# Kernel optimization log

Measured on AMD Instinct MI355X. Metric: run time of the kernel, lower is better.

## Reference

```python
import jax, jax.numpy as jnp
import numpy as np

B, S, D, H = 2, 2048, 1024, 16
DEPTH = D // H


def setup_inputs() -> dict:
    key = jax.random.key(0)
    ks = jax.random.split(key, 6)
    q = jax.random.normal(ks[0], (B, S, D), dtype=jnp.float32)
    k = jax.random.normal(ks[1], (B, S, D), dtype=jnp.float32)
    v = jax.random.normal(ks[2], (B, S, D), dtype=jnp.float32)
    # causal mask, broadcastable to [B, H, S, S]
    mask = jnp.tril(jnp.ones((S, S), dtype=bool))[None, None, :, :]
    wq = jax.random.normal(ks[3], (D, D), dtype=jnp.float32)
    wk = jax.random.normal(ks[4], (D, D), dtype=jnp.float32)
    wv = jax.random.normal(ks[5], (D, D), dtype=jnp.float32)
    return {"q": q, "k": k, "v": v, "mask": mask, "wq": wq, "wk": wk, "wv": wv}


def _split_heads(x):
    # [B, S, D] -> [B, H, S, depth]
    return x.reshape(x.shape[0], -1, H, DEPTH).transpose(0, 2, 1, 3)


def reference(q, k, v, mask, wq, wk, wv):
    q = _split_heads(q @ wq)
    k = _split_heads(k @ wk)
    v = _split_heads(v @ wv)
    scale = jnp.sqrt(jnp.float32(DEPTH))
    # [B, H, S, S]
    scores = jnp.einsum("bhqd,bhkd->bhqk", q, k) / scale
    scores = jnp.where(mask, scores, jnp.float32(-8.0))
    scores = scores - jnp.max(scores, axis=-1, keepdims=True)
    attn = jax.nn.softmax(scores, axis=-1)
    out = jnp.einsum("bhqk,bhkd->bhqd", attn, v)
    # [B, H, S, depth] -> [B, S, D]
    return out.transpose(0, 2, 1, 3).reshape(out.shape[0], -1, D)
```

## Files before the change

kernel.cpp:

```cpp
#include <hip/hip_runtime.h>
#include <hip/hip_bf16.h>

#define B_  2
#define S_  2048
#define D_  1024
#define H_  16
#define DH_ 64

typedef __attribute__((ext_vector_type(8)))  short  short8;
typedef __attribute__((ext_vector_type(4)))  short  short4b;
typedef __attribute__((ext_vector_type(16))) float  f32x16;

#define MFMA32(A,B,C) __builtin_amdgcn_mfma_f32_32x32x16_bf16(A,B,C,0,0,0)

static __device__ __forceinline__ short bf16b(float x) {
    __hip_bfloat16 h = __float2bfloat16(x);
    return *(short*)&h;
}
static __device__ __forceinline__ float bf16tof(short s) {
    union { unsigned u; float f; } cv;
    cv.u = ((unsigned)(unsigned short)s) << 16;
    return cv.f;
}
static __device__ __forceinline__ void gl2lds(const short* g, short* l) {
    __builtin_amdgcn_global_load_lds(
        (const __attribute__((address_space(1))) unsigned int*)g,
        (__attribute__((address_space(3))) unsigned int*)l, 16, 0, 0);
}
static __device__ __forceinline__ unsigned cvtpk(float a, float b) {
    unsigned r;
    asm("v_cvt_pk_bf16_f32 %0, %1, %2" : "=v"(r) : "v"(a), "v"(b));
    return r;
}
static __device__ __forceinline__ void pl32swap(unsigned &a, unsigned &b) {
    asm volatile("v_permlane32_swap_b32 %0, %1" : "+v"(a), "+v"(b));
}

__global__ __launch_bounds__(256)
void conv_all(const float* __restrict__ q, const float* __restrict__ k,
              const float* __restrict__ v,
              const float* __restrict__ wq, const float* __restrict__ wk,
              const float* __restrict__ wv, char* __restrict__ ws) {
    __shared__ short HiT[64][80];
    __shared__ short LoT[64][80];
    const int bid = blockIdx.x;
    const int t   = threadIdx.x;
    if (bid < 12288) {
        const int z   = bid >> 12;
        const int xb  = bid & 4095;
        const float* src = z == 0 ? q : z == 1 ? k : v;
        short* hi = (short*)(ws + (size_t)z * 16777216);
        short* lo = hi + 4194304;
        const int i = (xb * 256 + t) * 4;
        float4 xv = *(const float4*)&src[i];
        const float* xf = (const float*)&xv;
        short4b h4, l4;
#pragma unroll
        for (int e = 0; e < 4; ++e) {
            short hb = bf16b(xf[e]);
            h4[e] = hb;
            l4[e] = bf16b(xf[e] - bf16tof(hb));
        }
        *(short4b*)&hi[i] = h4;
        *(short4b*)&lo[i] = l4;
        return;
    }
    const int wid = bid - 12288;
    const int z   = wid >> 8;
    const int rem = wid & 255;
    const int k0  = (rem & 15) << 6, n0 = (rem >> 4) << 6;
    const float* w = z == 0 ? wq : z == 1 ? wk : wv;
    short* oh = (short*)(ws + 50331648 + (size_t)z * 4194304);
    short* ol = oh + 1048576;

    const int kr = t >> 2, c4 = (t & 3) * 16;
    const float* srow = w + (size_t)(k0 + kr) * 1024 + n0 + c4;
#pragma unroll
    for (int u = 0; u < 16; u += 4) {
        float4 f = *(const float4*)&srow[u];
        const float* ff = (const float*)&f;
#pragma unroll
        for (int e = 0; e < 4; ++e) {
            int nl = c4 + u + e;
            short hb = bf16b(ff[e]);
            HiT[nl][kr] = hb;
            LoT[nl][kr] = bf16b(ff[e] - bf16tof(hb));
        }
    }
    __syncthreads();
    const int nl = t >> 2, kc = (t & 3) * 16;
    size_t off = (size_t)(n0 + nl) * 1024 + k0 + kc;
    *(short8*)&oh[off]     = *(const short8*)&HiT[nl][kc];
    *(short8*)&oh[off + 8] = *(const short8*)&HiT[nl][kc + 8];
    *(short8*)&ol[off]     = *(const short8*)&LoT[nl][kc];
    *(short8*)&ol[off + 8] = *(const short8*)&LoT[nl][kc + 8];
}

#define QAH_ 0
#define QAL_ 4096
#define QBH_ 8192
#define QBL_ 12288

__global__ __launch_bounds__(512, 2)
void proj_mfma(const short* __restrict__ xh0, const short* __restrict__ xl0,
               const short* __restrict__ xh1, const short* __restrict__ xl1,
               const short* __restrict__ xh2, const short* __restrict__ xl2,
               const short* __restrict__ wh0, const short* __restrict__ wl0,
               const short* __restrict__ wh1, const short* __restrict__ wl1,
               const short* __restrict__ wh2, const short* __restrict__ wl2,
               short* __restrict__ qh, short* __restrict__ ql,
               short* __restrict__ kh, short* __restrict__ kl,
               short* __restrict__ vt) {
    __shared__ __align__(16) short lds[65536];
    const int z  = blockIdx.z;
    const int m0 = blockIdx.y * 256;
    const int n0 = blockIdx.x * 256;
    const int t = threadIdx.x, lane = t & 63, w = t >> 6;
    const int l31 = lane & 31, hh = lane >> 5;
    const int wr = w >> 2, wc = w & 3;

    const short* xh = z == 0 ? xh0 : z == 1 ? xh1 : xh2;
    const short* xl = z == 0 ? xl0 : z == 1 ? xl1 : xl2;
    const short* wh = z == 0 ? wh0 : z == 1 ? wh1 : wh2;
    const short* wl = z == 0 ? wl0 : z == 1 ? wl1 : wl2;

    const int c    = (w << 6) | lane;
    const int rowS = c >> 1, pq = c & 1;
    const int pqs8 = (pq ^ ((rowS >> 2) & 1)) * 8;
    const short* gAh = xh + (size_t)(m0 + rowS) * 1024 + pqs8;
    const short* gAl = xl + (size_t)(m0 + rowS) * 1024 + pqs8;
    const short* gBh = wh + (size_t)(n0 + rowS) * 1024 + pqs8;
    const short* gBl = wl + (size_t)(n0 + rowS) * 1024 + pqs8;
    const int wS = w << 9;

    const int co = ((hh ^ ((l31 >> 2) & 1)) << 3);
    int rA[4], rB[2];
#pragma unroll
    for (int p = 0; p < 4; ++p) rA[p] = (wr * 128 + p * 32 + l31) * 16 + co;
#pragma unroll
    for (int n = 0; n < 2; ++n) rB[n] = (wc * 64 + n * 32 + l31) * 16 + co;

    f32x16 acc[4][2] = {};

    gl2lds(gAh,      &lds[QAH_ + wS]);
    gl2lds(gBh,      &lds[QBH_ + wS]);
    gl2lds(gAl,      &lds[QAL_ + wS]);
    gl2lds(gBl,      &lds[QBL_ + wS]);
    gl2lds(gAh + 16, &lds[16384 + QAH_ + wS]);
    gl2lds(gBh + 16, &lds[16384 + QBH_ + wS]);
    gl2lds(gAl + 16, &lds[16384 + QAL_ + wS]);
    gl2lds(gBl + 16, &lds[16384 + QBL_ + wS]);
    asm volatile("s_waitcnt vmcnt(4)" ::: "memory");
    __builtin_amdgcn_s_barrier();

#define PHASE_MFMA(PA, PB)                                                    \
    acc[PA][0] = MFMA32(ah0, bh0k, acc[PA][0]);                               \
    acc[PA][1] = MFMA32(ah0, bh1k, acc[PA][1]);                               \
    acc[PB][0] = MFMA32(ah1, bh0k, acc[PB][0]);                               \
    acc[PB][1] = MFMA32(ah1, bh1k, acc[PB][1]);                               \
    acc[PA][0] = MFMA32(ah0, bl0k, acc[PA][0]);                               \
    acc[PA][1] = MFMA32(ah0, bl1k, acc[PA][1]);                               \
    acc[PB][0] = MFMA32(ah1, bl0k, acc[PB][0]);                               \
    acc[PB][1] = MFMA32(ah1, bl1k, acc[PB][1]);                               \
    acc[PA][0] = MFMA32(al0, bh0k, acc[PA][0]);                               \
    acc[PA][1] = MFMA32(al0, bh1k, acc[PA][1]);                               \
    acc[PB][0] = MFMA32(al1, bh0k, acc[PB][0]);                               \
    acc[PB][1] = MFMA32(al1, bh1k, acc[PB][1]);

    for (int kt = 0; kt < 32; ++kt) {
        const int tb = (kt & 1) << 15;
        const int nb = 32768 - tb;
        const int nk = (kt + 1) * 32;
        const bool st = (kt < 31);

        short8 bh0k, bh1k, bl0k, bl1k, ah0, ah1, al0, al1;

        __builtin_amdgcn_sched_barrier(0);
        bh0k = *(const short8*)&lds[tb + QBH_ + rB[0]];
        bh1k = *(const short8*)&lds[tb + QBH_ + rB[1]];
        bl0k = *(const short8*)&lds[tb + QBL_ + rB[0]];
        bl1k = *(const short8*)&lds[tb + QBL_ + rB[1]];
        ah0  = *(const short8*)&lds[tb + QAH_ + rA[0]];
        ah1  = *(const short8*)&lds[tb + QAH_ + rA[1]];
        al0  = *(const short8*)&lds[tb + QAL_ + rA[0]];
        al1  = *(const short8*)&lds[tb + QAL_ + rA[1]];
        if (st) { gl2lds(gAh + nk, &lds[nb + QAH_ + wS]);
                  gl2lds(gBh + nk, &lds[nb + QBH_ + wS]); }
        __builtin_amdgcn_s_barrier();
        asm volatile("s_waitcnt lgkmcnt(0)" ::: "memory");
        __builtin_amdgcn_sched_barrier(0);
        __builtin_amdgcn_s_setprio(1);
        PHASE_MFMA(0, 1)
        __builtin_amdgcn_s_setprio(0);
        __builtin_amdgcn_sched_barrier(0);
        __builtin_amdgcn_s_barrier();

        __builtin_amdgcn_sched_barrier(0);
        ah0 = *(const short8*)&lds[tb + QAH_ + rA[2]];
        ah1 = *(const short8*)&lds[tb + QAH_ + rA[3]];
        al0 = *(const short8*)&lds[tb + QAL_ + rA[2]];
        al1 = *(const short8*)&lds[tb + QAL_ + rA[3]];
        if (st) { gl2lds(gAl + nk, &lds[nb + QAL_ + wS]);
                  gl2lds(gBl + nk, &lds[nb + QBL_ + wS]);
                  asm volatile("s_waitcnt vmcnt(4)" ::: "memory");
        } else {  asm volatile("s_waitcnt vmcnt(0)" ::: "memory"); }
        __builtin_amdgcn_s_barrier();
        asm volatile("s_waitcnt lgkmcnt(0)" ::: "memory");
        __builtin_amdgcn_sched_barrier(0);
        __builtin_amdgcn_s_setprio(1);
        PHASE_MFMA(2, 3)
        __builtin_amdgcn_s_setprio(0);
        __builtin_amdgcn_sched_barrier(0);
        __builtin_amdgcn_s_barrier();

        __builtin_amdgcn_sched_barrier(0);
        bh0k = *(const short8*)&lds[tb + 16384 + QBH_ + rB[0]];
        bh1k = *(const short8*)&lds[tb + 16384 + QBH_ + rB[1]];
        bl0k = *(const short8*)&lds[tb + 16384 + QBL_ + rB[0]];
        bl1k = *(const short8*)&lds[tb + 16384 + QBL_ + rB[1]];
        ah0  = *(const short8*)&lds[tb + 16384 + QAH_ + rA[0]];
        ah1  = *(const short8*)&lds[tb + 16384 + QAH_ + rA[1]];
        al0  = *(const short8*)&lds[tb + 16384 + QAL_ + rA[0]];
        al1  = *(const short8*)&lds[tb + 16384 + QAL_ + rA[1]];
        if (st) { gl2lds(gAh + nk + 16, &lds[nb + 16384 + QAH_ + wS]);
                  gl2lds(gBh + nk + 16, &lds[nb + 16384 + QBH_ + wS]); }
        __builtin_amdgcn_s_barrier();
        asm volatile("s_waitcnt lgkmcnt(0)" ::: "memory");
        __builtin_amdgcn_sched_barrier(0);
        __builtin_amdgcn_s_setprio(1);
        PHASE_MFMA(0, 1)
        __builtin_amdgcn_s_setprio(0);
        __builtin_amdgcn_sched_barrier(0);
        __builtin_amdgcn_s_barrier();

        __builtin_amdgcn_sched_barrier(0);
        ah0 = *(const short8*)&lds[tb + 16384 + QAH_ + rA[2]];
        ah1 = *(const short8*)&lds[tb + 16384 + QAH_ + rA[3]];
        al0 = *(const short8*)&lds[tb + 16384 + QAL_ + rA[2]];
        al1 = *(const short8*)&lds[tb + 16384 + QAL_ + rA[3]];
        if (st) { gl2lds(gAl + nk + 16, &lds[nb + 16384 + QAL_ + wS]);
                  gl2lds(gBl + nk + 16, &lds[nb + 16384 + QBL_ + wS]);
                  asm volatile("s_waitcnt vmcnt(4)" ::: "memory"); }
        __builtin_amdgcn_s_barrier();
        asm volatile("s_waitcnt lgkmcnt(0)" ::: "memory");
        __builtin_amdgcn_sched_barrier(0);
        __builtin_amdgcn_s_setprio(1);
        PHASE_MFMA(2, 3)
        __builtin_amdgcn_s_setprio(0);
        __builtin_amdgcn_sched_barrier(0);
        __builtin_amdgcn_s_barrier();
    }
#undef PHASE_MFMA

    const int bb = m0 >> 11;
    const int sbase = (m0 & 2047) + wr * 128;
    if (z < 2) {
        short* oh = z == 0 ? qh : kh;
        short* ol = z == 0 ? ql : kl;
        const float qs = (z == 0) ? 0.125f : 1.0f;
#pragma unroll
        for (int p = 0; p < 4; ++p)
#pragma unroll
        for (int nt = 0; nt < 2; ++nt) {
            int n_g = n0 + wc * 64 + nt * 32 + l31;
            int h = n_g >> 6, d = n_g & 63;
#pragma unroll
            for (int r = 0; r < 16; ++r) {
                int s = sbase + p * 32 + (r & 3) + 8 * (r >> 2) + 4 * hh;
                size_t off = (((size_t)(bb * 16 + h) * 2048 + s) << 6) + d;
                float a = acc[p][nt][r] * qs;
                short hb = bf16b(a);
                oh[off] = hb;
                ol[off] = bf16b(a - bf16tof(hb));
            }
        }
    } else {
#pragma unroll
        for (int p = 0; p < 4; ++p)
#pragma unroll
        for (int nt = 0; nt < 2; ++nt) {
            int n_g = n0 + wc * 64 + nt * 32 + l31;
            int h = n_g >> 6, d = n_g & 63;
            size_t vbase = ((size_t)(bb * 16 + h) * 64 + d) * 2048;
#pragma unroll
            for (int r2 = 0; r2 < 4; ++r2) {
                int s0 = sbase + p * 32 + 8 * r2 + 4 * hh;
                short4b pk;
#pragma unroll
                for (int a2 = 0; a2 < 4; ++a2)
                    pk[a2] = bf16b(acc[p][nt][r2 * 4 + a2]);
                *(short4b*)&vt[vbase + s0] = pk;
            }
        }
    }
}

__global__ __launch_bounds__(256, 2)
void attn_mfma(const short* __restrict__ Qhi, const short* __restrict__ Qlo,
               const short* __restrict__ Khi, const short* __restrict__ Klo,
               const short* __restrict__ Vt,  float* __restrict__ out) {
    __shared__ __align__(16) short SBUF[24576];
    __shared__ float svp[4][64];
    __shared__ float svs[64];
#define KhiS (SBUF)
#define KloS (SBUF + 8192)
#define VtS  (SBUF + 16384)

    const int t     = threadIdx.x;
    const int lane  = t & 63;
    const int w     = t >> 6;
    const int l31   = lane & 31;
    const int hh    = lane >> 5;
    const int bh    = blockIdx.x;
    const int yy    = blockIdx.y;
    const int qt    = (yy < 8) ? yy : 23 - yy;
    const int q0    = qt * 128;
    const int myq   = q0 + w * 32 + l31;
    const int myq_min = q0 + w * 32;
    const int ktend = 2 * qt + 2;

    const size_t basebh = (size_t)bh * S_ * DH_;

    {
        const int s_begin = ktend * 64;
        float part = 0.f;
        const short* vrow = Vt + basebh + (size_t)lane * S_;
        for (int s = s_begin + w * 8; s < S_; s += 32) {
            short8 vv = *(const short8*)&vrow[s];
#pragma unroll
            for (int e = 0; e < 8; ++e) part += bf16tof(vv[e]);
        }
        svp[w][lane] = part;
    }
    __syncthreads();
    if (t < 64)
        svs[t] = svp[0][t] + svp[1][t] + svp[2][t] + svp[3][t];

    short8 qh[4], ql[4];
    {
        const short* qr = Qhi + basebh + (size_t)myq * DH_;
        const short* lr = Qlo + basebh + (size_t)myq * DH_;
#pragma unroll
        for (int kf = 0; kf < 4; ++kf) {
            int dofs = kf * 16 + hh * 8;
            qh[kf] = *(const short8*)(qr + dofs);
            ql[kf] = *(const short8*)(lr + dofs);
        }
    }

    const int i1 = (w << 6) | lane;
    const int i2 = 256 + i1;
    const int r1 = i1 >> 3, c1 = (i1 & 7) ^ (r1 & 7);
    const int r2 = i2 >> 3, c2 = (i2 & 7) ^ (r2 & 7);
    const short* gKh1 = Khi + basebh + (size_t)r1 * 64 + c1 * 8;
    const short* gKh2 = Khi + basebh + (size_t)r2 * 64 + c2 * 8;
    const short* gKl1 = Klo + basebh + (size_t)r1 * 64 + c1 * 8;
    const short* gKl2 = Klo + basebh + (size_t)r2 * 64 + c2 * 8;
    const short* gV1  = Vt  + basebh + (size_t)r1 * S_ + c1 * 8;
    const short* gV2  = Vt  + basebh + (size_t)r2 * S_ + c2 * 8;
    const int wub = w << 9;

#define ASTAGE(KT, BUF) do {                                                  \
        const int ka_ = (KT) * 4096, va_ = (KT) * 64, bo_ = (BUF) * 4096;     \
        gl2lds(gKh1 + ka_, &KhiS[bo_ + wub]);                                 \
        gl2lds(gKh2 + ka_, &KhiS[bo_ + 2048 + wub]);                          \
        gl2lds(gKl1 + ka_, &KloS[bo_ + wub]);                                 \
        gl2lds(gKl2 + ka_, &KloS[bo_ + 2048 + wub]);                          \
        gl2lds(gV1  + va_, &VtS [bo_ + wub]);                                 \
        gl2lds(gV2  + va_, &VtS [bo_ + 2048 + wub]);                          \
    } while (0)

    float m_run = -INFINITY, l_run = 0.f;
    f32x16 oT0 = {}, oT1 = {};

    const int sw0 = l31 & 7;

    ASTAGE(0, 0);

    for (int kt = 0; kt < ktend; ++kt) {
        const int bo = (kt & 1) << 12;
        asm volatile("s_waitcnt vmcnt(0)" ::: "memory");
        __builtin_amdgcn_s_barrier();
        __builtin_amdgcn_sched_barrier(0);
        if (kt + 1 < ktend)
            ASTAGE(kt + 1, (kt & 1) ^ 1);
        __builtin_amdgcn_sched_barrier(0);

        f32x16 acc0 = {}, acc1 = {};
        __builtin_amdgcn_s_setprio(1);
#pragma unroll
        for (int kf = 0; kf < 4; ++kf) {
            const int cs = ((2 * kf + hh) ^ sw0) << 3;
            short8 k0h = *(const short8*)&KhiS[bo + l31 * 64 + cs];
            short8 k0l = *(const short8*)&KloS[bo + l31 * 64 + cs];
            short8 k1h = *(const short8*)&KhiS[bo + (l31 + 32) * 64 + cs];
            short8 k1l = *(const short8*)&KloS[bo + (l31 + 32) * 64 + cs];
            acc0 = MFMA32(k0h, qh[kf], acc0);
            acc0 = MFMA32(k0h, ql[kf], acc0);
            acc0 = MFMA32(k0l, qh[kf], acc0);
            acc1 = MFMA32(k1h, qh[kf], acc1);
            acc1 = MFMA32(k1h, ql[kf], acc1);
            acc1 = MFMA32(k1l, qh[kf], acc1);
        }
        __builtin_amdgcn_s_setprio(0);

        float vals[32];
        float tmax;
        if (kt * 64 + 63 <= myq_min) {
            float t0 = -INFINITY, t1 = -INFINITY;
#pragma unroll
            for (int r = 0; r < 16; ++r) {
                vals[r]      = acc0[r];
                vals[16 + r] = acc1[r];
                t0 = fmaxf(t0, acc0[r]);
                t1 = fmaxf(t1, acc1[r]);
            }
            tmax = fmaxf(t0, t1);
        } else {
            tmax = -INFINITY;
#pragma unroll
            for (int r = 0; r < 16; ++r) {
                int key0 = kt * 64 + ((r & 3) + 8 * (r >> 2) + 4 * hh);
                float v0 = (key0 <= myq)      ? acc0[r] : -8.0f;
                float v1 = (key0 + 32 <= myq) ? acc1[r] : -8.0f;
                vals[r] = v0;
                vals[16 + r] = v1;
                tmax = fmaxf(tmax, fmaxf(v0, v1));
            }
        }
        tmax = fmaxf(tmax, __shfl_xor(tmax, 32, 64));
        const bool defer = __all(tmax <= m_run + 8.0f);
        if (!defer) {
            float mnew  = fmaxf(m_run, tmax);
            float alpha = __expf(m_run - mnew);
            l_run *= alpha;
#pragma unroll
            for (int r = 0; r < 16; ++r) { oT0[r] *= alpha; oT1[r] *= alpha; }
            m_run = mnew;
        }
        float psum = 0.f;
        unsigned cw[16];
#pragma unroll
        for (int tt = 0; tt < 16; ++tt) {
            float p0 = __expf(vals[2 * tt]     - m_run);
            float p1 = __expf(vals[2 * tt + 1] - m_run);
            psum += p0 + p1;
            cw[tt] = cvtpk(p0, p1);
        }
        psum += __shfl_xor(psum, 32, 64);
        l_run += psum;

        __builtin_amdgcn_s_setprio(1);
#pragma unroll
        for (int kf = 0; kf < 4; ++kf) {
            unsigned w0 = cw[4 * kf],     w1 = cw[4 * kf + 1];
            unsigned w2 = cw[4 * kf + 2], w3 = cw[4 * kf + 3];
            pl32swap(w0, w2);
            pl32swap(w1, w3);
            union { unsigned u[4]; short8 s8; } pu;
            pu.u[0] = w0; pu.u[1] = w1; pu.u[2] = w2; pu.u[3] = w3;
            const int cs = ((2 * kf + hh) ^ sw0) << 3;
            short8 v0 = *(const short8*)&VtS[bo + l31 * 64 + cs];
            short8 v1 = *(const short8*)&VtS[bo + (l31 + 32) * 64 + cs];
            oT0 = MFMA32(v0, pu.s8, oT0);
            oT1 = MFMA32(v1, pu.s8, oT1);
        }
        __builtin_amdgcn_s_setprio(0);
        __builtin_amdgcn_sched_barrier(0);
    }
#undef ASTAGE

    {
        float mfin = fmaxf(m_run, -8.0f);
        float aa   = __expf(m_run - mfin);
        float e8   = __expf(-8.0f - mfin);
        float nrem = (float)(S_ - ktend * 64);
        float lfin = l_run * aa + nrem * e8;
        float inv  = 1.0f / lfin;
#pragma unroll
        for (int r = 0; r < 16; ++r) {
            int dim0 = (r & 3) + 8 * (r >> 2) + 4 * hh;
            oT0[r] = (oT0[r] * aa + e8 * svs[dim0])      * inv;
            oT1[r] = (oT1[r] * aa + e8 * svs[dim0 + 32]) * inv;
        }
    }

    __syncthreads();
    float* Ob = (float*)SBUF + w * 2176;
#pragma unroll
    for (int r = 0; r < 16; ++r) {
        int dim0 = (r & 3) + 8 * (r >> 2) + 4 * hh;
        Ob[l31 * 68 + dim0]      = oT0[r];
        Ob[l31 * 68 + dim0 + 32] = oT1[r];
    }
    {
        const int qq = lane >> 1;
        const int ch = (lane & 1) * 32;
        const float* src = Ob + qq * 68 + ch;
        const int b  = bh >> 4;
        const int h  = bh & 15;
        float* dst = out + ((size_t)b * S_ + (q0 + w * 32 + qq)) * D_ + h * 64 + ch;
#pragma unroll
        for (int c = 0; c < 32; c += 4)
            *(float4*)(dst + c) = *(const float4*)(src + c);
    }
#undef KhiS
#undef KloS
#undef VtS
}

extern "C" void kernel_launch(void* const* d_in, const int* in_sizes, int n_in,
                              void* d_out, int out_size, void* d_ws, size_t ws_size,
                              hipStream_t stream) {
    const float* q  = (const float*)d_in[0];
    const float* k  = (const float*)d_in[1];
    const float* v  = (const float*)d_in[2];
    const float* wq = (const float*)d_in[4];
    const float* wk = (const float*)d_in[5];
    const float* wv = (const float*)d_in[6];
    float* out = (float*)d_out;

    char* ws = (char*)d_ws;
    const short* XH[3] = {(short*)ws, (short*)(ws + 16777216), (short*)(ws + 33554432)};
    const short* XL[3] = {XH[0] + 4194304, XH[1] + 4194304, XH[2] + 4194304};
    const short* WH[3] = {(short*)(ws + 50331648), (short*)(ws + 54525952), (short*)(ws + 58720256)};
    const short* WL[3] = {WH[0] + 1048576, WH[1] + 1048576, WH[2] + 1048576};

    short *Qhi, *Qlo, *Khi, *Klo, *Vt;
    if (ws_size >= (size_t)104857600) {
        Qhi = (short*)(ws + 62914560);
        Qlo = (short*)(ws + 71303168);
        Khi = (short*)(ws + 79691776);
        Klo = (short*)(ws + 88080384);
        Vt  = (short*)(ws + 96468992);
    } else {
        Qhi = (short*)d_in[0]; Qlo = Qhi + 4194304;
        Khi = (short*)d_in[1]; Klo = Khi + 4194304;
        Vt  = (short*)d_in[2];
    }

    conv_all<<<dim3(13056), 256, 0, stream>>>(q, k, v, wq, wk, wv, ws);

    proj_mfma<<<dim3(4, 16, 3), 512, 0, stream>>>(
        XH[0], XL[0], XH[1], XL[1], XH[2], XL[2],
        WH[0], WL[0], WH[1], WL[1], WH[2], WL[2],
        Qhi, Qlo, Khi, Klo, Vt);

    attn_mfma<<<dim3(32, 16), 256, 0, stream>>>(Qhi, Qlo, Khi, Klo, Vt, out);
}
```

Measured before the change: 267.3 us.

## Restructure projection GEMM LDS tiles to full 32-wide k rows with new swizzle

Changes the LDS layout of the split-bf16 projection GEMM so each staged row holds a full 32-element k slice (four 8-element chunks, XOR-swizzled by row) instead of two separate 16-wide halves. Global-to-LDS copies now read 64 contiguous bytes per row, and the prefetch issue is redistributed across the phases. The old partial vmcnt(4) waits are replaced by one full vmcnt(0) wait at the end of each k-step. This aims for more coalesced global loads and fewer LDS bank conflicts, at the cost of less overlap between the prefetch and the final MFMA phase.

```diff
diff --git a/kernel.cpp b/kernel.cpp
--- a/kernel.cpp
+++ b/kernel.cpp
@@ -96,10 +96,10 @@
     *(short8*)&ol[off + 8] = *(const short8*)&LoT[nl][kc + 8];
 }
 
-#define QAH_ 0
-#define QAL_ 4096
-#define QBH_ 8192
-#define QBL_ 12288
+#define AH_ 0
+#define AL_ 8192
+#define BH_ 16384
+#define BL_ 24576
 
 __global__ __launch_bounds__(512, 2)
 void proj_mfma(const short* __restrict__ xh0, const short* __restrict__ xl0,
@@ -124,33 +124,35 @@
     const short* wh = z == 0 ? wh0 : z == 1 ? wh1 : wh2;
     const short* wl = z == 0 ? wl0 : z == 1 ? wl1 : wl2;
 
-    const int c    = (w << 6) | lane;
-    const int rowS = c >> 1, pq = c & 1;
-    const int pqs8 = (pq ^ ((rowS >> 2) & 1)) * 8;
-    const short* gAh = xh + (size_t)(m0 + rowS) * 1024 + pqs8;
-    const short* gAl = xl + (size_t)(m0 + rowS) * 1024 + pqs8;
-    const short* gBh = wh + (size_t)(n0 + rowS) * 1024 + pqs8;
-    const short* gBl = wl + (size_t)(n0 + rowS) * 1024 + pqs8;
-    const int wS = w << 9;
-
-    const int co = ((hh ^ ((l31 >> 2) & 1)) << 3);
+    const short* gs[8];
+    short*       ld8[8];
+#pragma unroll
+    for (int j = 0; j < 8; ++j) {
+        const int arr = j >> 1;
+        const int cc  = t + ((j & 1) << 9);
+        const int row = cc >> 2, p = cc & 3;
+        const int kc  = p ^ ((row & 3) ^ ((row >> 2) & 3));
+        const short* base = arr == 0 ? xh : arr == 1 ? xl : arr == 2 ? wh : wl;
+        const int r0g = (arr < 2) ? m0 : n0;
+        gs[j]  = base + (size_t)(r0g + row) * 1024 + kc * 8;
+        ld8[j] = &lds[arr * 8192 + ((j & 1) << 12) + (w << 9)];
+    }
+
+    const int swl = (l31 & 3) ^ ((l31 >> 2) & 3);
+    const int co0 = (hh ^ swl) << 3;
+    const int co1 = ((2 | hh) ^ swl) << 3;
     int rA[4], rB[2];
 #pragma unroll
-    for (int p = 0; p < 4; ++p) rA[p] = (wr * 128 + p * 32 + l31) * 16 + co;
-#pragma unroll
-    for (int n = 0; n < 2; ++n) rB[n] = (wc * 64 + n * 32 + l31) * 16 + co;
+    for (int p = 0; p < 4; ++p) rA[p] = (wr * 128 + p * 32 + l31) * 32;
+#pragma unroll
+    for (int n = 0; n < 2; ++n) rB[n] = (wc * 64 + n * 32 + l31) * 32;
 
     f32x16 acc[4][2] = {};
 
-    gl2lds(gAh,      &lds[QAH_ + wS]);
-    gl2lds(gBh,      &lds[QBH_ + wS]);
-    gl2lds(gAl,      &lds[QAL_ + wS]);
-    gl2lds(gBl,      &lds[QBL_ + wS]);
-    gl2lds(gAh + 16, &lds[16384 + QAH_ + wS]);
-    gl2lds(gBh + 16, &lds[16384 + QBH_ + wS]);
-    gl2lds(gAl + 16, &lds[16384 + QAL_ + wS]);
-    gl2lds(gBl + 16, &lds[16384 + QBL_ + wS]);
-    asm volatile("s_waitcnt vmcnt(4)" ::: "memory");
+#pragma unroll
+    for (int j = 0; j < 8; ++j)
+        gl2lds(gs[j], ld8[j]);
+    asm volatile("s_waitcnt vmcnt(0)" ::: "memory");
     __builtin_amdgcn_s_barrier();
 
 #define PHASE_MFMA(PA, PB)                                                    \
@@ -169,23 +171,23 @@
 
     for (int kt = 0; kt < 32; ++kt) {
         const int tb = (kt & 1) << 15;
-        const int nb = 32768 - tb;
+        const int nbo = 32768 - tb;
         const int nk = (kt + 1) * 32;
         const bool st = (kt < 31);
 
         short8 bh0k, bh1k, bl0k, bl1k, ah0, ah1, al0, al1;
 
         __builtin_amdgcn_sched_barrier(0);
-        bh0k = *(const short8*)&lds[tb + QBH_ + rB[0]];
-        bh1k = *(const short8*)&lds[tb + QBH_ + rB[1]];
-        bl0k = *(const short8*)&lds[tb + QBL_ + rB[0]];
-        bl1k = *(const short8*)&lds[tb + QBL_ + rB[1]];
-        ah0  = *(const short8*)&lds[tb + QAH_ + rA[0]];
-        ah1  = *(const short8*)&lds[tb + QAH_ + rA[1]];
-        al0  = *(const short8*)&lds[tb + QAL_ + rA[0]];
-        al1  = *(const short8*)&lds[tb + QAL_ + rA[1]];
-        if (st) { gl2lds(gAh + nk, &lds[nb + QAH_ + wS]);
-                  gl2lds(gBh + nk, &lds[nb + QBH_ + wS]); }
+        bh0k = *(const short8*)&lds[tb + BH_ + rB[0] + co0];
+        bh1k = *(const short8*)&lds[tb + BH_ + rB[1] + co0];
+        bl0k = *(const short8*)&lds[tb + BL_ + rB[0] + co0];
+        bl1k = *(const short8*)&lds[tb + BL_ + rB[1] + co0];
+        ah0  = *(const short8*)&lds[tb + AH_ + rA[0] + co0];
+        ah1  = *(const short8*)&lds[tb + AH_ + rA[1] + co0];
+        al0  = *(const short8*)&lds[tb + AL_ + rA[0] + co0];
+        al1  = *(const short8*)&lds[tb + AL_ + rA[1] + co0];
+        if (st) { gl2lds(gs[0] + nk, ld8[0] + nbo);
+                  gl2lds(gs[1] + nk, ld8[1] + nbo); }
         __builtin_amdgcn_s_barrier();
         asm volatile("s_waitcnt lgkmcnt(0)" ::: "memory");
         __builtin_amdgcn_sched_barrier(0);
@@ -196,14 +198,12 @@
         __builtin_amdgcn_s_barrier();
 
         __builtin_amdgcn_sched_barrier(0);
-        ah0 = *(const short8*)&lds[tb + QAH_ + rA[2]];
-        ah1 = *(const short8*)&lds[tb + QAH_ + rA[3]];
-        al0 = *(const short8*)&lds[tb + QAL_ + rA[2]];
-        al1 = *(const short8*)&lds[tb + QAL_ + rA[3]];
-        if (st) { gl2lds(gAl + nk, &lds[nb + QAL_ + wS]);
-                  gl2lds(gBl + nk, &lds[nb + QBL_ + wS]);
-                  asm volatile("s_waitcnt vmcnt(4)" ::: "memory");
-        } else {  asm volatile("s_waitcnt vmcnt(0)" ::: "memory"); }
+        ah0 = *(const short8*)&lds[tb + AH_ + rA[2] + co0];
+        ah1 = *(const short8*)&lds[tb + AH_ + rA[3] + co0];
+        al0 = *(const short8*)&lds[tb + AL_ + rA[2] + co0];
+        al1 = *(const short8*)&lds[tb + AL_ + rA[3] + co0];
+        if (st) { gl2lds(gs[2] + nk, ld8[2] + nbo);
+                  gl2lds(gs[3] + nk, ld8[3] + nbo); }
         __builtin_amdgcn_s_barrier();
         asm volatile("s_waitcnt lgkmcnt(0)" ::: "memory");
         __builtin_amdgcn_sched_barrier(0);
@@ -214,16 +214,18 @@
         __builtin_amdgcn_s_barrier();
 
         __builtin_amdgcn_sched_barrier(0);
-        bh0k = *(const short8*)&lds[tb + 16384 + QBH_ + rB[0]];
-        bh1k = *(const short8*)&lds[tb + 16384 + QBH_ + rB[1]];
-        bl0k = *(const short8*)&lds[tb + 16384 + QBL_ + rB[0]];
-        bl1k = *(const short8*)&lds[tb + 16384 + QBL_ + rB[1]];
-        ah0  = *(const short8*)&lds[tb + 16384 + QAH_ + rA[0]];
-        ah1  = *(const short8*)&lds[tb + 16384 + QAH_ + rA[1]];
-        al0  = *(const short8*)&lds[tb + 16384 + QAL_ + rA[0]];
-        al1  = *(const short8*)&lds[tb + 16384 + QAL_ + rA[1]];
-        if (st) { gl2lds(gAh + nk + 16, &lds[nb + 16384 + QAH_ + wS]);
-                  gl2lds(gBh + nk + 16, &lds[nb + 16384 + QBH_ + wS]); }
+        bh0k = *(const short8*)&lds[tb + BH_ + rB[0] + co1];
+        bh1k = *(const short8*)&lds[tb + BH_ + rB[1] + co1];
+        bl0k = *(const short8*)&lds[tb + BL_ + rB[0] + co1];
+        bl1k = *(const short8*)&lds[tb + BL_ + rB[1] + co1];
+        ah0  = *(const short8*)&lds[tb + AH_ + rA[0] + co1];
+        ah1  = *(const short8*)&lds[tb + AH_ + rA[1] + co1];
+        al0  = *(const short8*)&lds[tb + AL_ + rA[0] + co1];
+        al1  = *(const short8*)&lds[tb + AL_ + rA[1] + co1];
+        if (st) { gl2lds(gs[4] + nk, ld8[4] + nbo);
+                  gl2lds(gs[5] + nk, ld8[5] + nbo);
+                  gl2lds(gs[6] + nk, ld8[6] + nbo);
+                  gl2lds(gs[7] + nk, ld8[7] + nbo); }
         __builtin_amdgcn_s_barrier();
         asm volatile("s_waitcnt lgkmcnt(0)" ::: "memory");
         __builtin_amdgcn_sched_barrier(0);
@@ -234,13 +236,10 @@
         __builtin_amdgcn_s_barrier();
 
         __builtin_amdgcn_sched_barrier(0);
-        ah0 = *(const short8*)&lds[tb + 16384 + QAH_ + rA[2]];
-        ah1 = *(const short8*)&lds[tb + 16384 + QAH_ + rA[3]];
-        al0 = *(const short8*)&lds[tb + 16384 + QAL_ + rA[2]];
-        al1 = *(const short8*)&lds[tb + 16384 + QAL_ + rA[3]];
-        if (st) { gl2lds(gAl + nk + 16, &lds[nb + 16384 + QAL_ + wS]);
-                  gl2lds(gBl + nk + 16, &lds[nb + 16384 + QBL_ + wS]);
-                  asm volatile("s_waitcnt vmcnt(4)" ::: "memory"); }
+        ah0 = *(const short8*)&lds[tb + AH_ + rA[2] + co1];
+        ah1 = *(const short8*)&lds[tb + AH_ + rA[3] + co1];
+        al0 = *(const short8*)&lds[tb + AL_ + rA[2] + co1];
+        al1 = *(const short8*)&lds[tb + AL_ + rA[3] + co1];
         __builtin_amdgcn_s_barrier();
         asm volatile("s_waitcnt lgkmcnt(0)" ::: "memory");
         __builtin_amdgcn_sched_barrier(0);
@@ -248,6 +247,7 @@
         PHASE_MFMA(2, 3)
         __builtin_amdgcn_s_setprio(0);
         __builtin_amdgcn_sched_barrier(0);
+        asm volatile("s_waitcnt vmcnt(0)" ::: "memory");
         __builtin_amdgcn_s_barrier();
     }
 #undef PHASE_MFMA
```

After: 266.4 us. No clear change (-0.3%).
